# Kernel optimization log

Measured on AMD Instinct MI355X. Metric: run time of the kernel, lower is better.

Reference implementation:

```python
import jax, jax.numpy as jnp
import numpy as np
import math

B, T, D = 8, 1024, 512
WS = 12          # window_size (top-k)
EPS = 1e-5       # BatchNorm eps (eval mode, running stats)
NEG = -1e9


def setup_inputs() -> dict:
    key = jax.random.key(0)
    ks = jax.random.split(key, 13)
    x = jax.random.normal(ks[0], (B, T, D), jnp.float32)
    conv1_w = jax.random.normal(ks[1], (512, 512, 5, 5), jnp.float32) / np.float32(np.sqrt(512 * 25))
    conv1_b = jax.random.normal(ks[2], (512,), jnp.float32) * 0.01
    bn1_g = jax.random.uniform(ks[3], (512,), jnp.float32, 0.5, 1.5)
    bn1_b = jax.random.normal(ks[4], (512,), jnp.float32) * 0.1
    bn1_m = jax.random.normal(ks[5], (512,), jnp.float32) * 0.1
    bn1_v = jax.random.uniform(ks[6], (512,), jnp.float32, 0.5, 1.5)
    conv2_w = jax.random.normal(ks[7], (512, 512, 5, 3), jnp.float32) / np.float32(np.sqrt(512 * 15))
    conv2_b = jax.random.normal(ks[8], (512,), jnp.float32) * 0.01
    bn2_g = jax.random.uniform(ks[9], (512,), jnp.float32, 0.5, 1.5)
    bn2_b = jax.random.normal(ks[10], (512,), jnp.float32) * 0.1
    bn2_m = jax.random.normal(ks[11], (512,), jnp.float32) * 0.1
    bn2_v = jax.random.uniform(ks[12], (512,), jnp.float32, 0.5, 1.5)
    return dict(x=x, conv1_w=conv1_w, conv1_b=conv1_b, bn1_g=bn1_g, bn1_b=bn1_b,
                bn1_m=bn1_m, bn1_v=bn1_v, conv2_w=conv2_w, conv2_b=conv2_b,
                bn2_g=bn2_g, bn2_b=bn2_b, bn2_m=bn2_m, bn2_v=bn2_v)


def _conv_nchw(h, w, b):
    # Conv2d padding=(2,0): pad height by 2 each side, no width padding.
    out = jax.lax.conv_general_dilated(h, w, window_strides=(1, 1),
                                       padding=((2, 2), (0, 0)),
                                       dimension_numbers=('NCHW', 'OIHW', 'NCHW'))
    return out + b[None, :, None, None]


def _bn(h, g, bt, m, v):
    # eval-mode BatchNorm2d with running stats
    inv = jax.lax.rsqrt(v + EPS)
    return (h - m[None, :, None, None]) * (g * inv)[None, :, None, None] + bt[None, :, None, None]


def _pool2(h):
    return jax.lax.reduce_window(h, -jnp.inf, jax.lax.max,
                                 (1, 1, 2, 2), (1, 1, 2, 2), 'VALID')


def reference(x, conv1_w, conv1_b, bn1_g, bn1_b, bn1_m, bn1_v,
              conv2_w, conv2_b, bn2_g, bn2_b, bn2_m, bn2_v):
    b, t, d = x.shape
    # masked local attention scores
    scores = jnp.einsum('btd,bsd->bts', x, x) / math.sqrt(d)  # [B,T,T]
    i = jnp.arange(t)[:, None]
    j = jnp.arange(t)[None, :]
    band = jnp.abs(j - i) <= (WS - 1)  # local band, width 2*WS-1
    scores = jnp.where(band[None], scores, NEG)
    # top-k window select, indices sorted ascending
    _, idx = jax.lax.top_k(scores, WS)           # [B,T,WS]
    ids = jnp.sort(idx, axis=-1)
    # batched gather: out[b,t,k,:] = x[b, ids[b,t,k], :]
    gathered = x[jnp.arange(b)[:, None, None], ids]  # [B,T,WS,D]
    h = gathered.transpose(0, 3, 1, 2)               # [B,512,T,WS]
    # conv encoder
    h = jax.nn.relu(_bn(_conv_nchw(h, conv1_w, conv1_b), bn1_g, bn1_b, bn1_m, bn1_v))
    h = _pool2(h)                                    # [B,512,T/2,4]
    h = jax.nn.relu(_bn(_conv_nchw(h, conv2_w, conv2_b), bn2_g, bn2_b, bn2_m, bn2_v))
    h = _pool2(h)                                    # [B,512,T/4,1]
    return jnp.squeeze(h)                            # [B,512,T/4]
```

## Files before the change

kernel.cpp:

```cpp
#include <hip/hip_runtime.h>
#include <hip/hip_bf16.h>

typedef short bf16x8 __attribute__((ext_vector_type(8)));
typedef float f32x16 __attribute__((ext_vector_type(16)));
typedef unsigned short u16;

__device__ __forceinline__ u16 f2bf(float v) {
    union { __hip_bfloat16 h; u16 u; } cv;
    cv.h = __float2bfloat16(v);
    return cv.u;
}

__device__ __forceinline__ void gld_lds16(const u16* g, u16* l) {
    __builtin_amdgcn_global_load_lds(
        (const __attribute__((address_space(1))) void*)g,
        (__attribute__((address_space(3))) void*)l, 16, 0, 0);
}

__global__ void prep_w1(const float* __restrict__ w, u16* __restrict__ o) {
    int idx = blockIdx.x * 256 + threadIdx.x;
    if (idx >= 25 * 512 * 512) return;
    int e = idx & 7, ocl = (idx >> 3) & 63, c = (idx >> 9) & 3;
    int ocs = (idx >> 11) & 7, T = idx >> 14;
    int icb = T / 25, tap = T - icb * 25;
    int ic = icb * 32 + c * 8 + e;
    int oc = ocs * 64 + ocl;
    int kh = tap / 5, kw = tap - kh * 5;
    o[idx] = f2bf(w[(((size_t)oc * 512 + ic) * 5 + kh) * 5 + kw]);
}

__global__ void prep_w2(const float* __restrict__ w, u16* __restrict__ o) {
    int idx = blockIdx.x * 256 + threadIdx.x;
    if (idx >= 15 * 512 * 512) return;
    int e = idx & 7, ocl = (idx >> 3) & 63, c = (idx >> 9) & 3;
    int ocs = (idx >> 11) & 7, T = idx >> 14;
    int icb = T / 15, tap = T - icb * 15;
    int ic = icb * 32 + c * 8 + e;
    int oc = ocs * 64 + ocl;
    int kh = tap / 3, kw = tap - kh * 3;
    o[idx] = f2bf(w[(((size_t)oc * 512 + ic) * 5 + kh) * 3 + kw]);
}

__global__ void prep_bn(const float* __restrict__ g, const float* __restrict__ b,
                        const float* __restrict__ m, const float* __restrict__ v,
                        float* __restrict__ scale, float* __restrict__ shift) {
    int i = blockIdx.x * 256 + threadIdx.x;
    if (i >= 512) return;
    float s = g[i] * rsqrtf(v[i] + 1e-5f);
    scale[i] = s;
    shift[i] = b[i] - m[i] * s;
}

__global__ void zero_pads(u16* __restrict__ gath, u16* __restrict__ pooled) {
    int idx = blockIdx.x * 256 + threadIdx.x;
    if (idx < 24576) {
        int w = idx % 12, r = idx / 12;
        int h4 = r & 3; r >>= 2;
        int cc = r & 63, b = r >> 6;
        int h = (h4 < 2) ? h4 : 1024 + h4;
        *(int4*)&gath[(((size_t)(b * 64 + cc)) * 12336 + h * 12 + w) * 8] =
            int4{0, 0, 0, 0};
    } else if (idx < 24576 + 8192) {
        int j = idx - 24576;
        int w = j & 3, r = j >> 2;
        int h4 = r & 3; r >>= 2;
        int cc = r & 63, b = r >> 6;
        int hp = (h4 < 2) ? h4 : 512 + h4;
        *(int4*)&pooled[(((size_t)(b * 64 + cc)) * 2064 + hp * 4 + w) * 8] =
            int4{0, 0, 0, 0};
    }
}

__global__ __launch_bounds__(256) void gather_topk(const float* __restrict__ x,
                                                   u16* __restrict__ g) {
    int bt = blockIdx.x;
    int b = bt >> 10, t = bt & 1023;
    const float* xb = x + (size_t)b * 1024 * 512;
    const float* xt = xb + (size_t)t * 512;
    __shared__ float xts[512];
    __shared__ float sc[23];
    __shared__ int sel[12];
    int tid = threadIdx.x;
    for (int i = tid; i < 512; i += 256) xts[i] = xt[i];
    __syncthreads();
    int j0 = t - 11; if (j0 < 0) j0 = 0;
    int j1 = t + 11; if (j1 > 1023) j1 = 1023;
    int C = j1 - j0 + 1;
    int wave = tid >> 6, lane = tid & 63;
    for (int c = wave; c < C; c += 4) {
        const float* xj = xb + (size_t)(j0 + c) * 512;
        double s = 0.0;
        #pragma unroll
        for (int e = 0; e < 8; ++e) {
            int d = lane * 8 + e;
            s += (double)xj[d] * (double)xts[d];
        }
        #pragma unroll
        for (int off = 32; off; off >>= 1) s += __shfl_xor(s, off, 64);
        if (lane == 0) sc[c] = (float)(s / 22.627416997969522);
    }
    __syncthreads();
    if (tid == 0) {
        int cnt = 0;
        for (int c = 0; c < C; ++c) {
            float v = sc[c];
            int r = 0;
            for (int k = 0; k < C; ++k) {
                float u = sc[k];
                r += (u > v) || (u == v && k < c);
            }
            if (r < 12) sel[cnt++] = j0 + c;
        }
    }
    __syncthreads();
    const size_t rowbase = (size_t)(t + 2) * 12;
    for (int i = tid; i < 768; i += 256) {
        int cc = i / 12, s = i - cc * 12;
        const float* src = xb + (size_t)sel[s] * 512 + cc * 8;
        float4 f0 = *(const float4*)src;
        float4 f1 = *(const float4*)(src + 4);
        u16 pk[8] = {f2bf(f0.x), f2bf(f0.y), f2bf(f0.z), f2bf(f0.w),
                     f2bf(f1.x), f2bf(f1.y), f2bf(f1.z), f2bf(f1.w)};
        *(int4*)&g[(((size_t)(b * 64 + cc)) * 12336 + rowbase + s) * 8] =
            *(const int4*)pk;
    }
}


template <int IN_W, int LOG_OW, int KH, int KW, int TH, int HTB, int MF32,
          int ARP, int PLANE, int CPX, bool POOL2E>
__global__ __launch_bounds__(512, 1) void conv_fused(
    const u16* __restrict__ A, const u16* __restrict__ Wt,
    const float* __restrict__ bias, const float* __restrict__ bnsc,
    const float* __restrict__ bnsh, void* __restrict__ outp) {
    constexpr int OW = 1 << LOG_OW;
    constexpr int TAPS = KH * KW;
    constexpr int JC = ARP / 64;
    constexpr int MFR = (32 >> LOG_OW) * IN_W;
    constexpr int SLAB = ARP * 8 + 32;
    __shared__ u16 As_l[8 * SLAB];

    const int tid = threadIdx.x;
    const int bid = blockIdx.x;
    const int lb = (bid & 7) * CPX + (bid >> 3);
    const int n0 = (lb & 1) * 256;
    const int mt = lb >> 1;
    const int b = mt / HTB;
    const int h0 = (mt % HTB) * TH;

    const int lane = tid & 63;
    const int wv = tid >> 6;
    const int wm = wv >> 2, wn = wv & 3;
    const int l31 = lane & 31, kgrp = lane >> 5;

    const int pos0 = wm * MF32 * 32 + l31;
    const int rowb0 = (pos0 >> LOG_OW) * IN_W + (pos0 & (OW - 1));
    const u16* aB = &As_l[kgrp * SLAB + rowb0 * 8];

    const int ocs = (lb & 1) * 4 + wn;
    const u16* wlane = Wt + (size_t)ocs * 2048 + kgrp * 512 + l31 * 8;

    const u16* gAh = A + (((size_t)b * 64) * PLANE + h0 * IN_W + lane) * 8;

    f32x16 acc[MF32][2];
    #pragma unroll
    for (int i = 0; i < MF32; ++i)
        #pragma unroll
        for (int j = 0; j < 2; ++j)
            acc[i][j] = f32x16{0.f,0.f,0.f,0.f,0.f,0.f,0.f,0.f,
                               0.f,0.f,0.f,0.f,0.f,0.f,0.f,0.f};

    #pragma unroll 1
    for (int q = wv; q < 8 * JC; q += 8) {
        int c8 = q / JC, j = q - c8 * JC;
        gld_lds16(gAh + ((size_t)(c8 * PLANE) + j * 64) * 8,
                  &As_l[c8 * SLAB + j * 512]);
    }
    bf16x8 wc0 = *(const bf16x8*)(wlane);
    bf16x8 wc1 = *(const bf16x8*)(wlane + 256);
    bf16x8 wc2 = *(const bf16x8*)(wlane + 1024);
    bf16x8 wc3 = *(const bf16x8*)(wlane + 1280);
    asm volatile("s_waitcnt vmcnt(0)" ::: "memory");
    __builtin_amdgcn_s_barrier();

    const u16* wsg = wlane + 16384;

    #pragma unroll 1
    for (int g = 0; g < 16; ++g) {
        const u16* aR = (g & 1) ? aB + 4 * SLAB : aB;
        #pragma unroll
        for (int t = 0; t < TAPS; ++t) {
            const u16* wS = wsg + (size_t)t * 16384;
            bf16x8 wn0 = *(const bf16x8*)(wS);
            bf16x8 wn1 = *(const bf16x8*)(wS + 256);
            bf16x8 wn2 = *(const bf16x8*)(wS + 1024);
            bf16x8 wn3 = *(const bf16x8*)(wS + 1280);
            const int kh_ = t / KW;
            const int toff = kh_ * IN_W + (t - kh_ * KW);
            __builtin_amdgcn_s_setprio(1);
            bf16x8 afr[MF32];
            #pragma unroll
            for (int mf = 0; mf < MF32; ++mf)
                afr[mf] = *(const bf16x8*)(aR + (toff + MFR * mf) * 8);
            #pragma unroll
            for (int mf = 0; mf < MF32; ++mf) {
                acc[mf][0] = __builtin_amdgcn_mfma_f32_32x32x16_bf16(
                    afr[mf], wc0, acc[mf][0], 0, 0, 0);
                acc[mf][1] = __builtin_amdgcn_mfma_f32_32x32x16_bf16(
                    afr[mf], wc1, acc[mf][1], 0, 0, 0);
            }
            #pragma unroll
            for (int mf = 0; mf < MF32; ++mf)
                afr[mf] = *(const bf16x8*)(aR + (toff + MFR * mf) * 8 + 2 * SLAB);
            #pragma unroll
            for (int mf = 0; mf < MF32; ++mf) {
                acc[mf][0] = __builtin_amdgcn_mfma_f32_32x32x16_bf16(
                    afr[mf], wc2, acc[mf][0], 0, 0, 0);
                acc[mf][1] = __builtin_amdgcn_mfma_f32_32x32x16_bf16(
                    afr[mf], wc3, acc[mf][1], 0, 0, 0);
            }
            __builtin_amdgcn_s_setprio(0);
            wc0 = wn0; wc1 = wn1; wc2 = wn2; wc3 = wn3;
        }
        wsg += (size_t)TAPS * 16384;
        if ((g & 1) && g < 15) {
            __builtin_amdgcn_s_barrier();
            const int chn = (g + 1) >> 1;
            #pragma unroll 1
            for (int q = wv; q < 8 * JC; q += 8) {
                int c8 = q / JC, j = q - c8 * JC;
                gld_lds16(gAh + ((size_t)((chn * 8 + c8) * PLANE) + j * 64) * 8,
                          &As_l[c8 * SLAB + j * 512]);
            }
            asm volatile("s_waitcnt vmcnt(0)" ::: "memory");
            __builtin_amdgcn_s_barrier();
        }
    }
    asm volatile("s_waitcnt vmcnt(0)" ::: "memory");

    #pragma unroll
    for (int nf = 0; nf < 2; ++nf) {
        const int oc = n0 + wn * 64 + nf * 32 + l31;
        const float scv = bnsc[oc], shv = bnsh[oc], bi = bias[oc];
        const float shh = fmaf(bi, scv, shv);
        #pragma unroll
        for (int mf = 0; mf < MF32; ++mf) {
            #pragma unroll
            for (int q = 0; q < 4; ++q) {
                if (!POOL2E) {
                    const int r0 = (q & 1) * 2 + (q >> 1) * 8;
                    float mx = fmaxf(
                        fmaxf(acc[mf][nf][r0], acc[mf][nf][r0 + 1]),
                        fmaxf(acc[mf][nf][r0 + 4], acc[mf][nf][r0 + 5]));
                    float v = fmaxf(fmaf(mx, scv, shh), 0.f);
                    const int row0 = (r0 & 3) + 8 * (r0 >> 2) + 4 * kgrp;
                    const int pos = wm * MF32 * 32 + mf * 32 + row0;
                    const int h = h0 + (pos >> LOG_OW);
                    const int w = pos & (OW - 1);
                    const int prow = (2 + (h >> 1)) * 4 + (w >> 1);
                    u16* o = (u16*)outp;
                    o[(((size_t)(b * 64 + (oc >> 3))) * 2064 + prow) * 8 +
                      (oc & 7)] = f2bf(v);
                } else {
                    const int r0 = q * 4;
                    float mx = fmaxf(
                        fmaxf(acc[mf][nf][r0], acc[mf][nf][r0 + 1]),
                        fmaxf(acc[mf][nf][r0 + 2], acc[mf][nf][r0 + 3]));
                    float v = fmaxf(fmaf(mx, scv, shh), 0.f);
                    const int row0 = 8 * (r0 >> 2) + 4 * kgrp;
                    const int pos = wm * 32 + row0;
                    const int pout = (h0 + (pos >> 1)) >> 1;
                    float* o = (float*)outp;
                    o[((size_t)(b * 512 + oc)) * 256 + pout] = v;
                }
            }
        }
    }
}

extern "C" void kernel_launch(void* const* d_in, const int* in_sizes, int n_in,
                              void* d_out, int out_size, void* d_ws, size_t ws_size,
                              hipStream_t stream) {
    const float* x  = (const float*)d_in[0];
    const float* w1 = (const float*)d_in[1];
    const float* b1 = (const float*)d_in[2];
    const float* g1 = (const float*)d_in[3];
    const float* be1 = (const float*)d_in[4];
    const float* m1 = (const float*)d_in[5];
    const float* v1 = (const float*)d_in[6];
    const float* w2 = (const float*)d_in[7];
    const float* b2 = (const float*)d_in[8];
    const float* g2 = (const float*)d_in[9];
    const float* be2 = (const float*)d_in[10];
    const float* m2 = (const float*)d_in[11];
    const float* v2 = (const float*)d_in[12];
    float* out = (float*)d_out;

    char* ws = (char*)d_ws;
    u16* gathered = (u16*)(ws);
    u16* w1t      = (u16*)(ws + 101056512);
    u16* w2t      = (u16*)(ws + 114163712);
    float* bn1s   = (float*)(ws + 122028032);
    float* bn1t   = bn1s + 512;
    float* bn2s   = bn1s + 1024;
    float* bn2t   = bn1s + 1536;
    u16* pooled1  = (u16*)(ws + 122036224);

    prep_w1<<<25600, 256, 0, stream>>>(w1, w1t);
    prep_w2<<<15360, 256, 0, stream>>>(w2, w2t);
    prep_bn<<<2, 256, 0, stream>>>(g1, be1, m1, v1, bn1s, bn1t);
    prep_bn<<<2, 256, 0, stream>>>(g2, be2, m2, v2, bn2s, bn2t);
    zero_pads<<<128, 256, 0, stream>>>(gathered, pooled1);
    gather_topk<<<8192, 256, 0, stream>>>(x, gathered);

    conv_fused<12, 3, 5, 5, 32, 32, 4, 448, 12336, 64, false>
        <<<512, 512, 0, stream>>>(gathered, w1t, b1, bn1s, bn1t, pooled1);
    conv_fused<4, 1, 5, 3, 32, 16, 1, 192, 2064, 32, true>
        <<<256, 512, 0, stream>>>(pooled1, w2t, b2, bn2s, bn2t, out);
}
```

Baseline: 888.1 us.

## Double-buffer LDS activation chunks and prefetch weights two taps ahead

The conv kernel now keeps two LDS buffers for the input-channel activation chunks. The next chunk is loaded with global_load_lds while MFMAs run on the current one, replacing the stall-and-barrier reload that happened every two groups. Weight fragments are now prefetched two taps ahead instead of one, which gives global loads more time to land. The cost is double the LDS footprint, more live registers for the extra weight fragments, and a partial vmcnt wait that depends on precise load ordering. The final iterations also prefetch weights past the last tap.

```diff
diff --git a/kernel.cpp b/kernel.cpp
--- a/kernel.cpp
+++ b/kernel.cpp
@@ -138,7 +138,7 @@
     constexpr int JC = ARP / 64;
     constexpr int MFR = (32 >> LOG_OW) * IN_W;
     constexpr int SLAB = ARP * 8 + 32;
-    __shared__ u16 As_l[8 * SLAB];
+    __shared__ u16 As_l[2][8 * SLAB];
 
     const int tid = threadIdx.x;
     const int bid = blockIdx.x;
@@ -155,7 +155,7 @@
 
     const int pos0 = wm * MF32 * 32 + l31;
     const int rowb0 = (pos0 >> LOG_OW) * IN_W + (pos0 & (OW - 1));
-    const u16* aB = &As_l[kgrp * SLAB + rowb0 * 8];
+    const int aoffb = kgrp * SLAB + rowb0 * 8;
 
     const int ocs = (lb & 1) * 4 + wn;
     const u16* wlane = Wt + (size_t)ocs * 2048 + kgrp * 512 + l31 * 8;
@@ -174,67 +174,74 @@
     for (int q = wv; q < 8 * JC; q += 8) {
         int c8 = q / JC, j = q - c8 * JC;
         gld_lds16(gAh + ((size_t)(c8 * PLANE) + j * 64) * 8,
-                  &As_l[c8 * SLAB + j * 512]);
+                  &As_l[0][c8 * SLAB + j * 512]);
     }
     bf16x8 wc0 = *(const bf16x8*)(wlane);
     bf16x8 wc1 = *(const bf16x8*)(wlane + 256);
     bf16x8 wc2 = *(const bf16x8*)(wlane + 1024);
     bf16x8 wc3 = *(const bf16x8*)(wlane + 1280);
+    bf16x8 wn0 = *(const bf16x8*)(wlane + 16384);
+    bf16x8 wn1 = *(const bf16x8*)(wlane + 16384 + 256);
+    bf16x8 wn2 = *(const bf16x8*)(wlane + 16384 + 1024);
+    bf16x8 wn3 = *(const bf16x8*)(wlane + 16384 + 1280);
+    const u16* wpf = wlane + 2 * 16384;
     asm volatile("s_waitcnt vmcnt(0)" ::: "memory");
     __builtin_amdgcn_s_barrier();
 
-    const u16* wsg = wlane + 16384;
-
     #pragma unroll 1
-    for (int g = 0; g < 16; ++g) {
-        const u16* aR = (g & 1) ? aB + 4 * SLAB : aB;
-        #pragma unroll
-        for (int t = 0; t < TAPS; ++t) {
-            const u16* wS = wsg + (size_t)t * 16384;
-            bf16x8 wn0 = *(const bf16x8*)(wS);
-            bf16x8 wn1 = *(const bf16x8*)(wS + 256);
-            bf16x8 wn2 = *(const bf16x8*)(wS + 1024);
-            bf16x8 wn3 = *(const bf16x8*)(wS + 1280);
-            const int kh_ = t / KW;
-            const int toff = kh_ * IN_W + (t - kh_ * KW);
-            __builtin_amdgcn_s_setprio(1);
-            bf16x8 afr[MF32];
-            #pragma unroll
-            for (int mf = 0; mf < MF32; ++mf)
-                afr[mf] = *(const bf16x8*)(aR + (toff + MFR * mf) * 8);
-            #pragma unroll
-            for (int mf = 0; mf < MF32; ++mf) {
-                acc[mf][0] = __builtin_amdgcn_mfma_f32_32x32x16_bf16(
-                    afr[mf], wc0, acc[mf][0], 0, 0, 0);
-                acc[mf][1] = __builtin_amdgcn_mfma_f32_32x32x16_bf16(
-                    afr[mf], wc1, acc[mf][1], 0, 0, 0);
-            }
-            #pragma unroll
-            for (int mf = 0; mf < MF32; ++mf)
-                afr[mf] = *(const bf16x8*)(aR + (toff + MFR * mf) * 8 + 2 * SLAB);
-            #pragma unroll
-            for (int mf = 0; mf < MF32; ++mf) {
-                acc[mf][0] = __builtin_amdgcn_mfma_f32_32x32x16_bf16(
-                    afr[mf], wc2, acc[mf][0], 0, 0, 0);
-                acc[mf][1] = __builtin_amdgcn_mfma_f32_32x32x16_bf16(
-                    afr[mf], wc3, acc[mf][1], 0, 0, 0);
-            }
-            __builtin_amdgcn_s_setprio(0);
-            wc0 = wn0; wc1 = wn1; wc2 = wn2; wc3 = wn3;
-        }
-        wsg += (size_t)TAPS * 16384;
-        if ((g & 1) && g < 15) {
-            __builtin_amdgcn_s_barrier();
-            const int chn = (g + 1) >> 1;
+    for (int cn = 0; cn < 8; ++cn) {
+        if (cn < 7) {
+            const int chn = cn + 1;
             #pragma unroll 1
             for (int q = wv; q < 8 * JC; q += 8) {
                 int c8 = q / JC, j = q - c8 * JC;
                 gld_lds16(gAh + ((size_t)((chn * 8 + c8) * PLANE) + j * 64) * 8,
-                          &As_l[c8 * SLAB + j * 512]);
+                          &As_l[chn & 1][c8 * SLAB + j * 512]);
             }
-            asm volatile("s_waitcnt vmcnt(0)" ::: "memory");
-            __builtin_amdgcn_s_barrier();
-        }
+        }
+        const u16* aBufc = &As_l[cn & 1][0] + aoffb;
+        #pragma unroll
+        for (int gh = 0; gh < 2; ++gh) {
+            const u16* aR = aBufc + gh * 4 * SLAB;
+            #pragma unroll
+            for (int t = 0; t < TAPS; ++t) {
+                bf16x8 wf0 = *(const bf16x8*)(wpf);
+                bf16x8 wf1 = *(const bf16x8*)(wpf + 256);
+                bf16x8 wf2 = *(const bf16x8*)(wpf + 1024);
+                bf16x8 wf3 = *(const bf16x8*)(wpf + 1280);
+                wpf += 16384;
+                const int kh_ = t / KW;
+                const int toff = kh_ * IN_W + (t - kh_ * KW);
+                __builtin_amdgcn_s_setprio(1);
+                bf16x8 afr[MF32];
+                #pragma unroll
+                for (int mf = 0; mf < MF32; ++mf)
+                    afr[mf] = *(const bf16x8*)(aR + (toff + MFR * mf) * 8);
+                #pragma unroll
+                for (int mf = 0; mf < MF32; ++mf) {
+                    acc[mf][0] = __builtin_amdgcn_mfma_f32_32x32x16_bf16(
+                        afr[mf], wc0, acc[mf][0], 0, 0, 0);
+                    acc[mf][1] = __builtin_amdgcn_mfma_f32_32x32x16_bf16(
+                        afr[mf], wc1, acc[mf][1], 0, 0, 0);
+                }
+                #pragma unroll
+                for (int mf = 0; mf < MF32; ++mf)
+                    afr[mf] = *(const bf16x8*)(aR + (toff + MFR * mf) * 8
+                                               + 2 * SLAB);
+                #pragma unroll
+                for (int mf = 0; mf < MF32; ++mf) {
+                    acc[mf][0] = __builtin_amdgcn_mfma_f32_32x32x16_bf16(
+                        afr[mf], wc2, acc[mf][0], 0, 0, 0);
+                    acc[mf][1] = __builtin_amdgcn_mfma_f32_32x32x16_bf16(
+                        afr[mf], wc3, acc[mf][1], 0, 0, 0);
+                }
+                __builtin_amdgcn_s_setprio(0);
+                wc0 = wn0; wc1 = wn1; wc2 = wn2; wc3 = wn3;
+                wn0 = wf0; wn1 = wf1; wn2 = wf2; wn3 = wf3;
+            }
+        }
+        asm volatile("s_waitcnt vmcnt(8)" ::: "memory");
+        __builtin_amdgcn_s_barrier();
     }
     asm volatile("s_waitcnt vmcnt(0)" ::: "memory");
 
```

Measured after the change: 889.5 us. No clear change (+0.2%).
